# Performance work log

Measured on AMD Instinct MI355X. Metric: run time of the kernel, lower is better.

Reference implementation:

```python
import jax, jax.numpy as jnp
import numpy as np

Q = 4096   # query_size = argument_size*relation_size*position_size = 32*16*8
L = 8192   # number of context rows


def setup_inputs() -> dict:
    key = jax.random.key(0)
    k1, k2, k3 = jax.random.split(key, 3)
    query = jax.random.normal(k1, (Q,), dtype=jnp.float32)
    context_vector = jax.random.normal(k2, (L, Q), dtype=jnp.float32)
    # torch Linear(2Q, Q, bias=False): weight shape [Q, 2Q], scaled init
    K_w = jax.random.normal(k3, (Q, 2 * Q), dtype=jnp.float32) / np.sqrt(2 * Q)
    return {"query": query, "context_vector": context_vector, "K_w": K_w}


def reference(query, context_vector, K_w):
    # score[l] = <context_vector[l], query>  -> [L]
    score = context_vector @ query
    attention = jax.nn.softmax(score, axis=0)          # softmax over L
    s_t = attention @ context_vector                    # [Q]
    gamma = jnp.concatenate([query, s_t])               # [2Q]
    return K_w @ gamma                                   # Linear(2Q -> Q), no bias
```

## Files before the change

### kernel.cpp

```cpp
#include <hip/hip_runtime.h>
#include <hip/hip_bf16.h>

#define Q 4096
#define L 8192

__global__ __launch_bounds__(256) void score_kernel(
    const float* __restrict__ ctx, const float* __restrict__ q,
    float* __restrict__ score)
{
    const int l = blockIdx.x;
    const float4* __restrict__ row = (const float4*)(ctx + (size_t)l * Q);
    const float4* __restrict__ qv  = (const float4*)q;

    float acc = 0.f;
    #pragma unroll
    for (int i = threadIdx.x; i < Q / 4; i += 256) {
        float4 a = row[i];
        float4 b = qv[i];
        acc = fmaf(a.x, b.x, acc);
        acc = fmaf(a.y, b.y, acc);
        acc = fmaf(a.z, b.z, acc);
        acc = fmaf(a.w, b.w, acc);
    }

    #pragma unroll
    for (int off = 32; off > 0; off >>= 1) acc += __shfl_down(acc, off, 64);

    __shared__ float red[4];
    const int lane = threadIdx.x & 63;
    const int wid  = threadIdx.x >> 6;
    if (lane == 0) red[wid] = acc;
    __syncthreads();
    if (threadIdx.x == 0)
        score[l] = red[0] + red[1] + red[2] + red[3];
}

__global__ __launch_bounds__(1024) void softmax_kernel(
    const float* __restrict__ score, float* __restrict__ att)
{
    __shared__ float redm[16];
    __shared__ float reds[16];
    const int tid  = threadIdx.x;
    const int lane = tid & 63;
    const int wid  = tid >> 6;

    float m = -3.4e38f;
    for (int i = tid; i < L; i += 1024) m = fmaxf(m, score[i]);
    #pragma unroll
    for (int off = 32; off > 0; off >>= 1) m = fmaxf(m, __shfl_down(m, off, 64));
    if (lane == 0) redm[wid] = m;
    __syncthreads();
    float mfull = redm[0];
    #pragma unroll
    for (int w = 1; w < 16; ++w) mfull = fmaxf(mfull, redm[w]);

    float s = 0.f;
    for (int i = tid; i < L; i += 1024) s += expf(score[i] - mfull);
    #pragma unroll
    for (int off = 32; off > 0; off >>= 1) s += __shfl_down(s, off, 64);
    if (lane == 0) reds[wid] = s;
    __syncthreads();
    float stot = 0.f;
    #pragma unroll
    for (int w = 0; w < 16; ++w) stot += reds[w];
    const float inv = 1.0f / stot;

    for (int i = tid; i < L; i += 1024) att[i] = expf(score[i] - mfull) * inv;
}

__global__ __launch_bounds__(256) void wsum_partial_kernel(
    const float* __restrict__ ctx, const float* __restrict__ att,
    float* __restrict__ partial)
{
    __shared__ float a_s[256];
    const int cq = blockIdx.x;
    const int cl = blockIdx.y;

    a_s[threadIdx.x] = att[cl * 256 + threadIdx.x];
    __syncthreads();

    const int col4 = cq * 256 + threadIdx.x;
    const float4* __restrict__ base = (const float4*)ctx;

    float4 acc = make_float4(0.f, 0.f, 0.f, 0.f);
    #pragma unroll 4
    for (int r = 0; r < 256; ++r) {
        const float a = a_s[r];
        float4 v = base[(size_t)(cl * 256 + r) * (Q / 4) + col4];
        acc.x = fmaf(a, v.x, acc.x);
        acc.y = fmaf(a, v.y, acc.y);
        acc.z = fmaf(a, v.z, acc.z);
        acc.w = fmaf(a, v.w, acc.w);
    }
    ((float4*)partial)[(size_t)cl * (Q / 4) + col4] = acc;
}

__global__ __launch_bounds__(256) void wsum_reduce_kernel(
    const float* __restrict__ partial, float* __restrict__ s_t)
{
    const int col4 = blockIdx.x * 256 + threadIdx.x;
    const float4* __restrict__ p = (const float4*)partial;
    float4 acc = make_float4(0.f, 0.f, 0.f, 0.f);
    #pragma unroll
    for (int cl = 0; cl < 32; ++cl) {
        float4 v = p[(size_t)cl * (Q / 4) + col4];
        acc.x += v.x; acc.y += v.y; acc.z += v.z; acc.w += v.w;
    }
    ((float4*)s_t)[col4] = acc;
}

__global__ __launch_bounds__(256) void out_mv_kernel(
    const float* __restrict__ Kw, const float* __restrict__ q,
    const float* __restrict__ s_t, float* __restrict__ out)
{
    const int i = blockIdx.x;
    const float4* __restrict__ row = (const float4*)(Kw + (size_t)i * (2 * Q));
    const float4* __restrict__ qv  = (const float4*)q;
    const float4* __restrict__ sv  = (const float4*)s_t;

    float acc = 0.f;
    #pragma unroll
    for (int j = threadIdx.x; j < Q / 4; j += 256) {
        float4 a = row[j];
        float4 b = qv[j];
        acc = fmaf(a.x, b.x, acc);
        acc = fmaf(a.y, b.y, acc);
        acc = fmaf(a.z, b.z, acc);
        acc = fmaf(a.w, b.w, acc);
    }
    #pragma unroll
    for (int j = threadIdx.x; j < Q / 4; j += 256) {
        float4 a = row[Q / 4 + j];
        float4 b = sv[j];
        acc = fmaf(a.x, b.x, acc);
        acc = fmaf(a.y, b.y, acc);
        acc = fmaf(a.z, b.z, acc);
        acc = fmaf(a.w, b.w, acc);
    }

    #pragma unroll
    for (int off = 32; off > 0; off >>= 1) acc += __shfl_down(acc, off, 64);

    __shared__ float red[4];
    const int lane = threadIdx.x & 63;
    const int wid  = threadIdx.x >> 6;
    if (lane == 0) red[wid] = acc;
    __syncthreads();
    if (threadIdx.x == 0)
        out[i] = red[0] + red[1] + red[2] + red[3];
}

extern "C" void kernel_launch(void* const* d_in, const int* in_sizes, int n_in,
                              void* d_out, int out_size, void* d_ws, size_t ws_size,
                              hipStream_t stream)
{
    const float* query = (const float*)d_in[0];
    const float* ctx   = (const float*)d_in[1];
    const float* Kw    = (const float*)d_in[2];
    float* out = (float*)d_out;

    float* ws      = (float*)d_ws;
    float* score   = ws;
    float* att     = ws + L;
    float* s_t     = ws + 2 * L;
    float* partial = ws + 2 * L + Q;

    score_kernel<<<L, 256, 0, stream>>>(ctx, query, score);
    softmax_kernel<<<1, 1024, 0, stream>>>(score, att);
    wsum_partial_kernel<<<dim3(4, 32), 256, 0, stream>>>(ctx, att, partial);
    wsum_reduce_kernel<<<4, 256, 0, stream>>>(partial, s_t);
    out_mv_kernel<<<Q, 256, 0, stream>>>(Kw, query, s_t, out);
}
```

Before: 79.43 us.

## Hoist K_w·query into score kernel and widen wsum grid to fill GPU

The K_w·query half of the output matvec moves into the first kernel, interleaved with the context-score rows, so it no longer waits behind softmax and the weighted sum. The weighted-sum kernel now launches 512 blocks of 64-row chunks instead of 128 blocks of 256 rows, which adds parallelism across CUs. In exchange, the reduce kernel has to sum 128 partials instead of 32. Softmax switches to the fast __expf intrinsic.

```diff
diff --git a/kernel.cpp b/kernel.cpp
--- a/kernel.cpp
+++ b/kernel.cpp
@@ -1,38 +1,49 @@
 #include <hip/hip_runtime.h>
-#include <hip/hip_bf16.h>
 
 #define Q 4096
 #define L 8192
 
-__global__ __launch_bounds__(256) void score_kernel(
-    const float* __restrict__ ctx, const float* __restrict__ q,
-    float* __restrict__ score)
+__global__ __launch_bounds__(256) void k1_kernel(
+    const float* __restrict__ qvec, const float* __restrict__ ctx,
+    const float* __restrict__ Kw, float* __restrict__ score,
+    float* __restrict__ out1)
 {
-    const int l = blockIdx.x;
-    const float4* __restrict__ row = (const float4*)(ctx + (size_t)l * Q);
-    const float4* __restrict__ qv  = (const float4*)q;
+    const int b   = blockIdx.x;
+    const int fam = b % 3;
+    const int g   = b / 3;
+    const int tid  = threadIdx.x;
+    const int lane = tid & 63;
+    const int wid  = tid >> 6;
 
+    const float4* __restrict__ row;
+    float* outp;
+    if (fam < 2) {
+        const int l = g * 2 + fam;
+        row  = (const float4*)(ctx + (size_t)l * Q);
+        outp = score + l;
+    } else {
+        row  = (const float4*)(Kw + (size_t)g * (2 * Q));
+        outp = out1 + g;
+    }
+
+    const float4* __restrict__ qv = (const float4*)qvec;
     float acc = 0.f;
     #pragma unroll
-    for (int i = threadIdx.x; i < Q / 4; i += 256) {
+    for (int i = tid; i < Q / 4; i += 256) {
         float4 a = row[i];
-        float4 b = qv[i];
-        acc = fmaf(a.x, b.x, acc);
-        acc = fmaf(a.y, b.y, acc);
-        acc = fmaf(a.z, b.z, acc);
-        acc = fmaf(a.w, b.w, acc);
+        float4 c = qv[i];
+        acc = fmaf(a.x, c.x, acc);
+        acc = fmaf(a.y, c.y, acc);
+        acc = fmaf(a.z, c.z, acc);
+        acc = fmaf(a.w, c.w, acc);
     }
-
     #pragma unroll
     for (int off = 32; off > 0; off >>= 1) acc += __shfl_down(acc, off, 64);
 
     __shared__ float red[4];
-    const int lane = threadIdx.x & 63;
-    const int wid  = threadIdx.x >> 6;
     if (lane == 0) red[wid] = acc;
     __syncthreads();
-    if (threadIdx.x == 0)
-        score[l] = red[0] + red[1] + red[2] + red[3];
+    if (tid == 0) *outp = red[0] + red[1] + red[2] + red[3];
 }
 
 __global__ __launch_bounds__(1024) void softmax_kernel(
@@ -50,104 +61,95 @@
     for (int off = 32; off > 0; off >>= 1) m = fmaxf(m, __shfl_down(m, off, 64));
     if (lane == 0) redm[wid] = m;
     __syncthreads();
-    float mfull = redm[0];
+    float M = redm[0];
     #pragma unroll
-    for (int w = 1; w < 16; ++w) mfull = fmaxf(mfull, redm[w]);
+    for (int w = 1; w < 16; ++w) M = fmaxf(M, redm[w]);
 
     float s = 0.f;
-    for (int i = tid; i < L; i += 1024) s += expf(score[i] - mfull);
+    for (int i = tid; i < L; i += 1024) s += __expf(score[i] - M);
     #pragma unroll
     for (int off = 32; off > 0; off >>= 1) s += __shfl_down(s, off, 64);
     if (lane == 0) reds[wid] = s;
     __syncthreads();
-    float stot = 0.f;
+    float Z = 0.f;
     #pragma unroll
-    for (int w = 0; w < 16; ++w) stot += reds[w];
-    const float inv = 1.0f / stot;
+    for (int w = 0; w < 16; ++w) Z += reds[w];
+    const float inv = 1.0f / Z;
 
-    for (int i = tid; i < L; i += 1024) att[i] = expf(score[i] - mfull) * inv;
+    for (int i = tid; i < L; i += 1024) att[i] = __expf(score[i] - M) * inv;
 }
 
-__global__ __launch_bounds__(256) void wsum_partial_kernel(
+__global__ __launch_bounds__(256) void wsum_kernel(
     const float* __restrict__ ctx, const float* __restrict__ att,
     float* __restrict__ partial)
 {
-    __shared__ float a_s[256];
-    const int cq = blockIdx.x;
-    const int cl = blockIdx.y;
+    __shared__ float att_s[128];
+    const int cc = blockIdx.x & 7;
+    const int rc = blockIdx.x >> 3;
+    const int tid = threadIdx.x;
+    const int rg  = tid >> 7;
+    const int col = cc * 128 + (tid & 127);
 
-    a_s[threadIdx.x] = att[cl * 256 + threadIdx.x];
+    if (tid < 128) att_s[tid] = att[rc * 128 + tid];
     __syncthreads();
 
-    const int col4 = cq * 256 + threadIdx.x;
-    const float4* __restrict__ base = (const float4*)ctx;
-
+    const float4* __restrict__ cb = (const float4*)ctx;
+    const int r0 = rc * 128 + rg * 64;
     float4 acc = make_float4(0.f, 0.f, 0.f, 0.f);
-    #pragma unroll 4
-    for (int r = 0; r < 256; ++r) {
-        const float a = a_s[r];
-        float4 v = base[(size_t)(cl * 256 + r) * (Q / 4) + col4];
+    #pragma unroll 8
+    for (int r = 0; r < 64; ++r) {
+        const float a = att_s[rg * 64 + r];
+        float4 v = cb[(size_t)(r0 + r) * (Q / 4) + col];
         acc.x = fmaf(a, v.x, acc.x);
         acc.y = fmaf(a, v.y, acc.y);
         acc.z = fmaf(a, v.z, acc.z);
         acc.w = fmaf(a, v.w, acc.w);
     }
-    ((float4*)partial)[(size_t)cl * (Q / 4) + col4] = acc;
+    ((float4*)partial)[(size_t)(rc * 2 + rg) * (Q / 4) + col] = acc;
 }
 
-__global__ __launch_bounds__(256) void wsum_reduce_kernel(
+__global__ __launch_bounds__(256) void reduce_kernel(
     const float* __restrict__ partial, float* __restrict__ s_t)
 {
-    const int col4 = blockIdx.x * 256 + threadIdx.x;
+    const int c4 = blockIdx.x * 256 + threadIdx.x;
     const float4* __restrict__ p = (const float4*)partial;
     float4 acc = make_float4(0.f, 0.f, 0.f, 0.f);
-    #pragma unroll
-    for (int cl = 0; cl < 32; ++cl) {
-        float4 v = p[(size_t)cl * (Q / 4) + col4];
+    #pragma unroll 8
+    for (int b = 0; b < 128; ++b) {
+        float4 v = p[(size_t)b * (Q / 4) + c4];
         acc.x += v.x; acc.y += v.y; acc.z += v.z; acc.w += v.w;
     }
-    ((float4*)s_t)[col4] = acc;
+    ((float4*)s_t)[c4] = acc;
 }
 
-__global__ __launch_bounds__(256) void out_mv_kernel(
-    const float* __restrict__ Kw, const float* __restrict__ q,
-    const float* __restrict__ s_t, float* __restrict__ out)
+__global__ __launch_bounds__(256) void k5_kernel(
+    const float* __restrict__ Kw, const float* __restrict__ s_t,
+    const float* __restrict__ out1, float* __restrict__ out)
 {
     const int i = blockIdx.x;
-    const float4* __restrict__ row = (const float4*)(Kw + (size_t)i * (2 * Q));
-    const float4* __restrict__ qv  = (const float4*)q;
+    const int tid  = threadIdx.x;
+    const int lane = tid & 63;
+    const int wid  = tid >> 6;
+    const float4* __restrict__ row = (const float4*)(Kw + (size_t)i * (2 * Q) + Q);
     const float4* __restrict__ sv  = (const float4*)s_t;
 
     float acc = 0.f;
     #pragma unroll
-    for (int j = threadIdx.x; j < Q / 4; j += 256) {
+    for (int j = tid; j < Q / 4; j += 256) {
         float4 a = row[j];
-        float4 b = qv[j];
-        acc = fmaf(a.x, b.x, acc);
-        acc = fmaf(a.y, b.y, acc);
-        acc = fmaf(a.z, b.z, acc);
-        acc = fmaf(a.w, b.w, acc);
+        float4 c = sv[j];
+        acc = fmaf(a.x, c.x, acc);
+        acc = fmaf(a.y, c.y, acc);
+        acc = fmaf(a.z, c.z, acc);
+        acc = fmaf(a.w, c.w, acc);
     }
-    #pragma unroll
-    for (int j = threadIdx.x; j < Q / 4; j += 256) {
-        float4 a = row[Q / 4 + j];
-        float4 b = sv[j];
-        acc = fmaf(a.x, b.x, acc);
-        acc = fmaf(a.y, b.y, acc);
-        acc = fmaf(a.z, b.z, acc);
-        acc = fmaf(a.w, b.w, acc);
-    }
-
     #pragma unroll
     for (int off = 32; off > 0; off >>= 1) acc += __shfl_down(acc, off, 64);
 
     __shared__ float red[4];
-    const int lane = threadIdx.x & 63;
-    const int wid  = threadIdx.x >> 6;
     if (lane == 0) red[wid] = acc;
     __syncthreads();
-    if (threadIdx.x == 0)
-        out[i] = red[0] + red[1] + red[2] + red[3];
+    if (tid == 0) out[i] = out1[i] + red[0] + red[1] + red[2] + red[3];
 }
 
 extern "C" void kernel_launch(void* const* d_in, const int* in_sizes, int n_in,
@@ -162,12 +164,13 @@
     float* ws      = (float*)d_ws;
     float* score   = ws;
     float* att     = ws + L;
-    float* s_t     = ws + 2 * L;
-    float* partial = ws + 2 * L + Q;
+    float* out1    = ws + 2 * L;
+    float* s_t     = ws + 2 * L + Q;
+    float* partial = ws + 2 * L + 2 * Q;
 
-    score_kernel<<<L, 256, 0, stream>>>(ctx, query, score);
+    k1_kernel<<<12288, 256, 0, stream>>>(query, ctx, Kw, score, out1);
     softmax_kernel<<<1, 1024, 0, stream>>>(score, att);
-    wsum_partial_kernel<<<dim3(4, 32), 256, 0, stream>>>(ctx, att, partial);
-    wsum_reduce_kernel<<<4, 256, 0, stream>>>(partial, s_t);
-    out_mv_kernel<<<Q, 256, 0, stream>>>(Kw, query, s_t, out);
+    wsum_kernel<<<512, 256, 0, stream>>>(ctx, att, partial);
+    reduce_kernel<<<4, 256, 0, stream>>>(partial, s_t);
+    k5_kernel<<<Q, 256, 0, stream>>>(Kw, s_t, out1, out);
 }
```

New measurement: 79.86 us. About the same (+0.6%).
